# Optimization experiments

Measured on AMD Instinct MI355X. Metric: run time of the kernel, lower is better.

## Reference

```python
import jax, jax.numpy as jnp
import numpy as np

N_HEADS = 16
ROPE_BASE = 10000.0


def _rope(x):
    # x: [B, L, H, Dh]; LLaMA-style rotate-half RoPE, applied over seq dim 1
    B, L, H, Dh = x.shape
    half = Dh // 2
    inv_freq = 1.0 / (ROPE_BASE ** (jnp.arange(0, half, dtype=jnp.float32) / half))
    ang = jnp.arange(L, dtype=jnp.float32)[:, None] * inv_freq[None, :]  # [L, half]
    cos = jnp.concatenate([jnp.cos(ang), jnp.cos(ang)], axis=-1).astype(x.dtype)  # [L, Dh]
    sin = jnp.concatenate([jnp.sin(ang), jnp.sin(ang)], axis=-1).astype(x.dtype)
    cos = cos[None, :, None, :]
    sin = sin[None, :, None, :]
    x1, x2 = x[..., :half], x[..., half:]
    rot = jnp.concatenate([-x2, x1], axis=-1)
    return x * cos + rot * sin


def setup_inputs() -> dict:
    key = jax.random.key(0)
    k1, k2, k3 = jax.random.split(key, 3)
    B, L, D = 2, 2048, 1024
    x = jax.random.normal(k1, (B, L, D), dtype=jnp.float32)
    w_qkv = jax.random.normal(k2, (3 * D, D), dtype=jnp.float32) * (D ** -0.5)
    w_out = jax.random.normal(k3, (D, D), dtype=jnp.float32) * (D ** -0.5)
    return {"x": x, "w_qkv": w_qkv, "w_out": w_out}


def reference(x, w_qkv, w_out):
    B, L, D = x.shape
    H = N_HEADS
    Dh = D // H
    qkv = jnp.einsum('bld,ed->ble', x, w_qkv)  # [B, L, 3D]
    q, k, v = jnp.split(qkv, 3, axis=-1)
    q = q.reshape(B, L, H, Dh)
    k = k.reshape(B, L, H, Dh)
    v = v.reshape(B, L, H, Dh)
    q = _rope(q)
    k = _rope(k)
    scale = 1.0 / jnp.sqrt(jnp.asarray(Dh, dtype=x.dtype))
    scores = jnp.einsum('blhd,bmhd->bhlm', q, k) * scale  # [B, H, L, L]
    attn = jax.nn.softmax(scores, axis=-1)
    out = jnp.einsum('bhlm,bmhd->blhd', attn, v).reshape(B, L, D)
    return jnp.einsum('bld,ed->ble', out, w_out)
```

## Files before the change

### kernel.cpp

```cpp
#include <hip/hip_runtime.h>
#include <hip/hip_bf16.h>
#include <stdint.h>


typedef __attribute__((ext_vector_type(8))) short short8;
typedef __attribute__((ext_vector_type(4))) float floatx4;
typedef __attribute__((ext_vector_type(16))) float floatx16;
typedef __attribute__((ext_vector_type(4))) int intx4;

#define BDIM 2
#define LDIM 2048
#define DDIM 1024
#define HDIM 16
#define DH 64
#define ML (BDIM * LDIM)

#define QSCALE 0.18033688011112042f
#define SMBIAS 16.0f

__device__ __forceinline__ uint16_t f2b(float x) {
  uint32_t b = __float_as_uint(x);
  b += 0x7FFFu + ((b >> 16) & 1u);
  return (uint16_t)(b >> 16);
}

__device__ __forceinline__ uint32_t pack2(float a, float b) {
  return (uint32_t)f2b(a) | ((uint32_t)f2b(b) << 16);
}

__device__ __forceinline__ uint32_t cvtpk(float lo, float hi) {
  uint32_t r;
  asm("v_cvt_pk_bf16_f32 %0, %1, %2" : "=v"(r) : "v"(lo), "v"(hi));
  return r;
}

#define PLSWAP(a, b) asm("v_permlane32_swap_b32 %0, %1" : "+v"(a), "+v"(b))

__device__ __forceinline__ void load_lds_16B(const uint16_t* g, uint16_t* l) {
  __builtin_amdgcn_global_load_lds(
      (const __attribute__((address_space(1))) void*)g,
      (__attribute__((address_space(3))) void*)l, 16, 0, 0);
}

#define WAIT_BAR(N) do {                                         \
    asm volatile("s_waitcnt vmcnt(" #N ")" ::: "memory");        \
    __builtin_amdgcn_sched_barrier(0);                           \
    __builtin_amdgcn_s_barrier();                                \
    asm volatile("" ::: "memory");                               \
    __builtin_amdgcn_sched_barrier(0);                           \
  } while (0)

union I4S8 { intx4 i; short8 s; };

__global__ void prep(const float* __restrict__ x, const float* __restrict__ wqkv,
                     const float* __restrict__ wout,
                     uint16_t* __restrict__ xb, uint16_t* __restrict__ wqkvb,
                     uint16_t* __restrict__ woutb,
                     float* __restrict__ cosT, float* __restrict__ sinT) {
  const int N0 = ML * DDIM / 4;
  const int N1 = 3 * DDIM * DDIM / 4;
  const int N2 = DDIM * DDIM / 4;
  int id = blockIdx.x * 256 + threadIdx.x;
  if (id < N0) {
    float4 v = ((const float4*)x)[id];
    ((uint2*)xb)[id] = make_uint2(pack2(v.x, v.y), pack2(v.z, v.w));
  } else if (id < N0 + N1) {
    int i = id - N0;
    float4 v = ((const float4*)wqkv)[i];
    ((uint2*)wqkvb)[i] = make_uint2(pack2(v.x, v.y), pack2(v.z, v.w));
  } else if (id < N0 + N1 + N2) {
    int i = id - N0 - N1;
    float4 v = ((const float4*)wout)[i];
    ((uint2*)woutb)[i] = make_uint2(pack2(v.x, v.y), pack2(v.z, v.w));
  } else {
    int i = id - N0 - N1 - N2;
    int l = i >> 5, f = i & 31;
    float invf = exp2f(-(float)f * (13.287712379549449f / 32.f));
    float ang = (float)l * invf;
    cosT[i] = cosf(ang);
    sinT[i] = sinf(ang);
  }
}

__device__ __forceinline__ void gemm_step(const uint16_t* __restrict__ as,
                                          const uint16_t* __restrict__ bs,
                                          int wr, int wc, int c0, int c1,
                                          floatx4 (&acc)[4][4]) {
  short8 a[4], b[4];
#pragma unroll
  for (int i = 0; i < 4; ++i)
    a[i] = *(const short8*)&as[(wr * 64 + i * 16 + c0) * 32 + c1 * 8];
#pragma unroll
  for (int j = 0; j < 4; ++j)
    b[j] = *(const short8*)&bs[(wc * 64 + j * 16 + c0) * 32 + c1 * 8];
#pragma unroll
  for (int i = 0; i < 4; ++i)
#pragma unroll
    for (int j = 0; j < 4; ++j)
      acc[i][j] = __builtin_amdgcn_mfma_f32_16x16x32_bf16(a[i], b[j], acc[i][j], 0, 0, 0);
}

#define GEMM_STAGE(BUF, K0) do {                                              \
    const uint16_t* ga = A + (size_t)(m0 + srow) * K + (K0) + scol;           \
    load_lds_16B(ga, &As[(BUF) * 4096 + t * 8]);                              \
    load_lds_16B(ga + (size_t)64 * K, &As[(BUF) * 4096 + 2048 + t * 8]);      \
    const uint16_t* gb = Bm + (size_t)(n0 + srow) * K + (K0) + scol;          \
    load_lds_16B(gb, &Bs[(BUF) * 4096 + t * 8]);                              \
    load_lds_16B(gb + (size_t)64 * K, &Bs[(BUF) * 4096 + 2048 + t * 8]);      \
  } while (0)

__global__ __launch_bounds__(256) void gemm_bt(const uint16_t* __restrict__ A,
                                               const uint16_t* __restrict__ Bm,
                                               float* __restrict__ C,
                                               int M, int N, int K) {
  __shared__ uint16_t As[3 * 4096];
  __shared__ uint16_t Bs[3 * 4096];
  const int m0 = blockIdx.x * 128;
  const int n0 = blockIdx.y * 128;
  const int t = threadIdx.x;
  const int lane = t & 63;
  const int w = t >> 6;
  const int wr = w >> 1, wc = w & 1;
  const int srow = t >> 2;
  const int scol = (t & 3) * 8;
  const int c0 = lane & 15, c1 = lane >> 4;

  floatx4 acc[4][4];
#pragma unroll
  for (int i = 0; i < 4; ++i)
#pragma unroll
    for (int j = 0; j < 4; ++j) acc[i][j] = (floatx4){0.f, 0.f, 0.f, 0.f};

  const int nk = K >> 5;
  GEMM_STAGE(0, 0);
  GEMM_STAGE(1, 32);
#pragma unroll 1
  for (int ki = 0; ki < nk - 1; ++ki) {
    WAIT_BAR(4);
    if (ki + 2 < nk) GEMM_STAGE((ki + 2) % 3, (ki + 2) * 32);
    gemm_step(&As[(ki % 3) * 4096], &Bs[(ki % 3) * 4096], wr, wc, c0, c1, acc);
  }
  WAIT_BAR(0);
  gemm_step(&As[((nk - 1) % 3) * 4096], &Bs[((nk - 1) % 3) * 4096], wr, wc, c0, c1, acc);

#pragma unroll
  for (int i = 0; i < 4; ++i)
#pragma unroll
    for (int j = 0; j < 4; ++j) {
      int row = m0 + wr * 64 + i * 16 + c1 * 4;
      int col = n0 + wc * 64 + j * 16 + c0;
      float* cp = C + (size_t)row * N + col;
#pragma unroll
      for (int r = 0; r < 4; ++r) cp[(size_t)r * N] = acc[i][j][r];
    }
}

__global__ __launch_bounds__(256) void gemm_qkv_rope(const uint16_t* __restrict__ A,
                                                     const uint16_t* __restrict__ Bm,
                                                     const float* __restrict__ cosT,
                                                     const float* __restrict__ sinT,
                                                     uint16_t* __restrict__ qr,
                                                     uint16_t* __restrict__ kr,
                                                     uint16_t* __restrict__ vT) {
  constexpr int K = DDIM;
  __shared__ uint16_t As[3 * 4096];
  __shared__ uint16_t Bs[3 * 4096];
  const int m0 = blockIdx.x * 128;
  const int n0 = blockIdx.y * 128;
  const int t = threadIdx.x;
  const int lane = t & 63;
  const int w = t >> 6;
  const int wr = w >> 1, wc = w & 1;
  const int srow = t >> 2;
  const int scol = (t & 3) * 8;
  const int c0 = lane & 15, c1 = lane >> 4;

  floatx4 acc[4][4];
#pragma unroll
  for (int i = 0; i < 4; ++i)
#pragma unroll
    for (int j = 0; j < 4; ++j) acc[i][j] = (floatx4){0.f, 0.f, 0.f, 0.f};

  const int nk = K >> 5;
  GEMM_STAGE(0, 0);
  GEMM_STAGE(1, 32);
#pragma unroll 1
  for (int ki = 0; ki < nk - 1; ++ki) {
    WAIT_BAR(4);
    if (ki + 2 < nk) GEMM_STAGE((ki + 2) % 3, (ki + 2) * 32);
    gemm_step(&As[(ki % 3) * 4096], &Bs[(ki % 3) * 4096], wr, wc, c0, c1, acc);
  }
  WAIT_BAR(0);
  gemm_step(&As[((nk - 1) % 3) * 4096], &Bs[((nk - 1) % 3) * 4096], wr, wc, c0, c1, acc);

#pragma unroll
  for (int j = 0; j < 4; ++j) {
    const int col = n0 + wc * 64 + j * 16 + c0;
    const int sec = col >> 10;
    const int e = col & 1023;
    const int h = e >> 6, dh = e & 63;
#pragma unroll
    for (int i = 0; i < 4; ++i) {
      const int row = m0 + wr * 64 + i * 16 + c1 * 4;
      const int bb = row >> 11;
      const int l = row & 2047;
      if (sec == 2) {
        uint16_t* vp = vT + ((size_t)((bb * HDIM + h) * DH + dh)) * LDIM + l;
#pragma unroll
        for (int r = 0; r < 4; ++r) vp[r] = f2b(acc[i][j][r]);
      } else {
        const float sgn = (dh < 32) ? -1.f : 1.f;
        const float sc = (sec == 0) ? QSCALE : 1.f;
        uint16_t* dp = (sec == 0 ? qr : kr) + ((size_t)((bb * HDIM + h) * LDIM + l)) * DH + dh;
        const int fi = l * 32 + (dh & 31);
#pragma unroll
        for (int r = 0; r < 4; ++r) {
          float cv = cosT[fi + r * 32];
          float sv = sinT[fi + r * 32];
          float o = (acc[i][j][r] * cv + sgn * acc[i][j ^ 2][r] * sv) * sc;
          dp[(size_t)r * DH] = f2b(o);
        }
      }
    }
  }
}


__device__ __forceinline__ void qk_phase(const uint16_t* __restrict__ kt,
                                         const int (&off)[2][4],
                                         const short8 (&qb)[4],
                                         floatx16& s0, floatx16& s1) {
  floatx16 z = (floatx16){-SMBIAS,-SMBIAS,-SMBIAS,-SMBIAS,-SMBIAS,-SMBIAS,-SMBIAS,-SMBIAS,
                          -SMBIAS,-SMBIAS,-SMBIAS,-SMBIAS,-SMBIAS,-SMBIAS,-SMBIAS,-SMBIAS};
  s0 = z; s1 = z;
  __builtin_amdgcn_s_setprio(1);
#pragma unroll
  for (int c = 0; c < 4; ++c) {
    short8 ka = *(const short8*)(kt + off[0][c]);
    s0 = __builtin_amdgcn_mfma_f32_32x32x16_bf16(ka, qb[c], s0, 0, 0, 0);
  }
#pragma unroll
  for (int c = 0; c < 4; ++c) {
    short8 ka = *(const short8*)(kt + off[1][c]);
    s1 = __builtin_amdgcn_mfma_f32_32x32x16_bf16(ka, qb[c], s1, 0, 0, 0);
  }
  __builtin_amdgcn_s_setprio(0);
}

__device__ __forceinline__ void sm_pv(const uint16_t* __restrict__ vt,
                                      const int (&off)[2][4],
                                      floatx16& s0, floatx16& s1,
                                      float& lsum,
                                      floatx16& acc0, floatx16& acc1) {
  float e[32];
#pragma unroll
  for (int r = 0; r < 16; ++r) e[r] = __builtin_amdgcn_exp2f(s0[r]);
#pragma unroll
  for (int r = 0; r < 16; ++r) e[16 + r] = __builtin_amdgcn_exp2f(s1[r]);
  float ts0 = 0.f, ts1 = 0.f, ts2 = 0.f, ts3 = 0.f;
#pragma unroll
  for (int r = 0; r < 8; ++r) {
    ts0 += e[r]; ts1 += e[8 + r]; ts2 += e[16 + r]; ts3 += e[24 + r];
  }
  lsum += (ts0 + ts1) + (ts2 + ts3);

  uint32_t w0 = cvtpk(e[0], e[1]),   w1 = cvtpk(e[2], e[3]);
  uint32_t w2 = cvtpk(e[4], e[5]),   w3 = cvtpk(e[6], e[7]);
  uint32_t w4 = cvtpk(e[8], e[9]),   w5 = cvtpk(e[10], e[11]);
  uint32_t w6 = cvtpk(e[12], e[13]), w7 = cvtpk(e[14], e[15]);
  uint32_t w8 = cvtpk(e[16], e[17]), w9 = cvtpk(e[18], e[19]);
  uint32_t wa = cvtpk(e[20], e[21]), wb = cvtpk(e[22], e[23]);
  uint32_t wc_ = cvtpk(e[24], e[25]), wd = cvtpk(e[26], e[27]);
  uint32_t we = cvtpk(e[28], e[29]), wf = cvtpk(e[30], e[31]);
  PLSWAP(w0, w2);  PLSWAP(w1, w3);
  PLSWAP(w4, w6);  PLSWAP(w5, w7);
  PLSWAP(w8, wa);  PLSWAP(w9, wb);
  PLSWAP(wc_, we); PLSWAP(wd, wf);
  I4S8 pf0, pf1, pf2, pf3;
  pf0.i = (intx4){(int)w0, (int)w1, (int)w2, (int)w3};
  pf1.i = (intx4){(int)w4, (int)w5, (int)w6, (int)w7};
  pf2.i = (intx4){(int)w8, (int)w9, (int)wa, (int)wb};
  pf3.i = (intx4){(int)wc_, (int)wd, (int)we, (int)wf};

  __builtin_amdgcn_s_setprio(1);
#pragma unroll
  for (int d = 0; d < 2; ++d) {
    floatx16& ac = d ? acc1 : acc0;
    ac = __builtin_amdgcn_mfma_f32_32x32x16_bf16(*(const short8*)(vt + off[d][0]), pf0.s, ac, 0, 0, 0);
    ac = __builtin_amdgcn_mfma_f32_32x32x16_bf16(*(const short8*)(vt + off[d][1]), pf1.s, ac, 0, 0, 0);
    ac = __builtin_amdgcn_mfma_f32_32x32x16_bf16(*(const short8*)(vt + off[d][2]), pf2.s, ac, 0, 0, 0);
    ac = __builtin_amdgcn_mfma_f32_32x32x16_bf16(*(const short8*)(vt + off[d][3]), pf3.s, ac, 0, 0, 0);
  }
  __builtin_amdgcn_s_setprio(0);
}

__global__ __launch_bounds__(256) void attn(const uint16_t* __restrict__ qr,
                                            const uint16_t* __restrict__ kr,
                                            const uint16_t* __restrict__ vT,
                                            uint16_t* __restrict__ out) {
  __shared__ uint16_t KsA[4 * 4096];
  __shared__ uint16_t VsA[4 * 4096];
  const int t = threadIdx.x, lane = t & 63, w = t >> 6;
  const int l31 = lane & 31, hi = lane >> 5;

  const int id = blockIdx.x;
  const int sw = (id & 7) * 64 + (id >> 3);
  const int bx = sw & 15;
  const int h = (sw >> 4) & 15;
  const int b = sw >> 8;

  const int bh = b * HDIM + h;
  const uint16_t* Qb = qr + (size_t)bh * LDIM * DH;
  const char* Kp = (const char*)(kr + (size_t)bh * LDIM * DH);
  const char* Vp = (const char*)(vT + (size_t)bh * DH * LDIM);

  const int srow = t >> 3;
  const int scsw = ((t & 7) * 16) ^ ((srow & 7) << 4);
  const char* kgs = Kp + (size_t)srow * 128 + scsw;
  const char* vgs = Vp + (size_t)srow * (LDIM * 2) + scsw;

#define STAGE(BUF, N) do {                                                     \
    uint16_t* kd = &KsA[(BUF) * 4096];                                         \
    uint16_t* vd = &VsA[(BUF) * 4096];                                         \
    load_lds_16B((const uint16_t*)(kgs + (size_t)(N) * 8192), &kd[t * 8]);     \
    load_lds_16B((const uint16_t*)(kgs + (size_t)(N) * 8192 + 4096), &kd[2048 + t * 8]); \
    load_lds_16B((const uint16_t*)(vgs + (size_t)(N) * 128), &vd[t * 8]);      \
    load_lds_16B((const uint16_t*)(vgs + (size_t)(N) * 128 + 2 * 32 * LDIM), &vd[2048 + t * 8]); \
  } while (0)

  const int q0 = bx * 128 + w * 32;
  short8 qb[4];
#pragma unroll
  for (int c = 0; c < 4; ++c)
    qb[c] = *(const short8*)&Qb[(size_t)(q0 + l31) * DH + c * 16 + hi * 8];

  const int swz = (l31 & 7) << 4;
  int off[2][4];
#pragma unroll
  for (int x = 0; x < 2; ++x)
#pragma unroll
    for (int c = 0; c < 4; ++c)
      off[x][c] = (x * 32 + l31) * 64 + (((c * 32 + hi * 16) ^ swz) >> 1);

  float lsum = 0.f;
  floatx16 acc0 = (floatx16){0.f,0.f,0.f,0.f,0.f,0.f,0.f,0.f,0.f,0.f,0.f,0.f,0.f,0.f,0.f,0.f};
  floatx16 acc1 = acc0;
  floatx16 sA0, sA1, sB0, sB1;

  STAGE(0, 0); STAGE(1, 1); STAGE(2, 2);
  WAIT_BAR(8);
  qk_phase(&KsA[0], off, qb, sA0, sA1);

#define BODY(n, CS0, CS1, NS0, NS1, WN) do {                                   \
    WAIT_BAR(WN);                                                              \
    if ((n) + 3 < 32) STAGE(((n) + 3) & 3, (n) + 3);                           \
    qk_phase(&KsA[(((n) + 1) & 3) * 4096], off, qb, NS0, NS1);                 \
    sm_pv(&VsA[((n) & 3) * 4096], off, CS0, CS1, lsum, acc0, acc1);            \
  } while (0)

#pragma unroll 1
  for (int n = 0; n < 30; n += 2) {
    BODY(n, sA0, sA1, sB0, sB1, 4);
    BODY(n + 1, sB0, sB1, sA0, sA1, 4);
  }
  BODY(30, sA0, sA1, sB0, sB1, 0);
  sm_pv(&VsA[3 * 4096], off, sB0, sB1, lsum, acc0, acc1);
#undef BODY
#undef STAGE

  float ltot = lsum + __shfl_xor(lsum, 32);
  float inv = 1.f / ltot;
  size_t orow = (size_t)(b * LDIM) + bx * 128 + w * 32 + l31;
  uint16_t* op = out + orow * DDIM + h * DH;
#pragma unroll
  for (int g = 0; g < 4; ++g) {
    *(uint2*)&op[8 * g + 4 * hi] =
        make_uint2(cvtpk(acc0[4 * g] * inv, acc0[4 * g + 1] * inv),
                   cvtpk(acc0[4 * g + 2] * inv, acc0[4 * g + 3] * inv));
    *(uint2*)&op[32 + 8 * g + 4 * hi] =
        make_uint2(cvtpk(acc1[4 * g] * inv, acc1[4 * g + 1] * inv),
                   cvtpk(acc1[4 * g + 2] * inv, acc1[4 * g + 3] * inv));
  }
}

static constexpr size_t OFF_XB    = 0;
static constexpr size_t OFF_WQKVB = (size_t)8 << 20;
static constexpr size_t OFF_WOUTB = (size_t)14 << 20;
static constexpr size_t OFF_QR    = (size_t)16 << 20;
static constexpr size_t OFF_KR    = (size_t)24 << 20;
static constexpr size_t OFF_VT    = (size_t)32 << 20;
static constexpr size_t OFF_AO    = (size_t)40 << 20;
static constexpr size_t OFF_COS   = (size_t)48 << 20;
static constexpr size_t OFF_SIN   = OFF_COS + ((size_t)256 << 10);

extern "C" void kernel_launch(void* const* d_in, const int* in_sizes, int n_in,
                              void* d_out, int out_size, void* d_ws, size_t ws_size,
                              hipStream_t stream) {
  const float* x     = (const float*)d_in[0];
  const float* w_qkv = (const float*)d_in[1];
  const float* w_out = (const float*)d_in[2];
  float* out = (float*)d_out;
  char* ws = (char*)d_ws;

  uint16_t* xb    = (uint16_t*)(ws + OFF_XB);
  uint16_t* wqkvb = (uint16_t*)(ws + OFF_WQKVB);
  uint16_t* woutb = (uint16_t*)(ws + OFF_WOUTB);
  uint16_t* qr    = (uint16_t*)(ws + OFF_QR);
  uint16_t* kr    = (uint16_t*)(ws + OFF_KR);
  uint16_t* vT    = (uint16_t*)(ws + OFF_VT);
  uint16_t* ao    = (uint16_t*)(ws + OFF_AO);
  float*    cosT  = (float*)(ws + OFF_COS);
  float*    sinT  = (float*)(ws + OFF_SIN);

  prep<<<8448, 256, 0, stream>>>(x, w_qkv, w_out, xb, wqkvb, woutb, cosT, sinT);

  gemm_qkv_rope<<<dim3(ML / 128, 3 * DDIM / 128), 256, 0, stream>>>(xb, wqkvb, cosT, sinT, qr, kr, vT);

  attn<<<512, 256, 0, stream>>>(qr, kr, vT, ao);

  gemm_bt<<<dim3(ML / 128, DDIM / 128), 256, 0, stream>>>(ao, woutb, out, ML, DDIM, DDIM);
}
```

Before: 116.0 us.

## Stage QKV epilogue through LDS for coalesced stores and swizzle GEMM block order

The QKV+RoPE GEMM epilogue now writes results into a padded shared-memory tile and then emits 16-byte coalesced stores to q, k and the transposed v, replacing scattered 2-byte global writes. Both GEMMs switch to a 1D grid with an XCD-aware block swizzle (id&7 mapping), so blocks sharing an A or B panel land on the same chiplet for better L2 reuse. The cost is extra LDS traffic and two barriers in the epilogue. The swizzle hardcodes the grid shapes (32 row tiles).

```diff
diff --git a/kernel.cpp b/kernel.cpp
--- a/kernel.cpp
+++ b/kernel.cpp
@@ -115,8 +115,10 @@
                                                int M, int N, int K) {
   __shared__ uint16_t As[3 * 4096];
   __shared__ uint16_t Bs[3 * 4096];
-  const int m0 = blockIdx.x * 128;
-  const int n0 = blockIdx.y * 128;
+  const int id = blockIdx.x;
+  const int sw = (id & 7) * (gridDim.x >> 3) + (id >> 3);
+  const int m0 = (sw & 31) * 128;
+  const int n0 = (sw >> 5) * 128;
   const int t = threadIdx.x;
   const int lane = t & 63;
   const int w = t >> 6;
@@ -163,10 +165,13 @@
                                                      uint16_t* __restrict__ kr,
                                                      uint16_t* __restrict__ vT) {
   constexpr int K = DDIM;
-  __shared__ uint16_t As[3 * 4096];
-  __shared__ uint16_t Bs[3 * 4096];
-  const int m0 = blockIdx.x * 128;
-  const int n0 = blockIdx.y * 128;
+  __shared__ uint16_t SH[6 * 4096];
+  uint16_t* As = SH;
+  uint16_t* Bs = SH + 3 * 4096;
+  const int id = blockIdx.x;
+  const int sw = (id & 7) * 96 + (id >> 3);
+  const int m0 = (sw & 31) * 128;
+  const int n0 = (sw >> 5) * 128;
   const int t = threadIdx.x;
   const int lane = t & 63;
   const int w = t >> 6;
@@ -193,35 +198,62 @@
   WAIT_BAR(0);
   gemm_step(&As[((nk - 1) % 3) * 4096], &Bs[((nk - 1) % 3) * 4096], wr, wc, c0, c1, acc);
 
-#pragma unroll
-  for (int j = 0; j < 4; ++j) {
-    const int col = n0 + wc * 64 + j * 16 + c0;
-    const int sec = col >> 10;
-    const int e = col & 1023;
-    const int h = e >> 6, dh = e & 63;
-#pragma unroll
-    for (int i = 0; i < 4; ++i) {
-      const int row = m0 + wr * 64 + i * 16 + c1 * 4;
-      const int bb = row >> 11;
-      const int l = row & 2047;
-      if (sec == 2) {
-        uint16_t* vp = vT + ((size_t)((bb * HDIM + h) * DH + dh)) * LDIM + l;
-#pragma unroll
-        for (int r = 0; r < 4; ++r) vp[r] = f2b(acc[i][j][r]);
-      } else {
-        const float sgn = (dh < 32) ? -1.f : 1.f;
-        const float sc = (sec == 0) ? QSCALE : 1.f;
-        uint16_t* dp = (sec == 0 ? qr : kr) + ((size_t)((bb * HDIM + h) * LDIM + l)) * DH + dh;
-        const int fi = l * 32 + (dh & 31);
+  __syncthreads();
+  uint16_t (*ep)[136] = (uint16_t (*)[136])SH;
+  const int sec = n0 >> 10;
+  const int bb = m0 >> 11;
+  const int l0 = m0 & 2047;
+
+  if (sec == 2) {
+#pragma unroll
+    for (int j = 0; j < 4; ++j) {
+      const int colL = wc * 64 + j * 16 + c0;
+#pragma unroll
+      for (int i = 0; i < 4; ++i) {
+        const int rowL = wr * 64 + i * 16 + c1 * 4;
+#pragma unroll
+        for (int r = 0; r < 4; ++r)
+          ep[colL][rowL + r] = f2b(acc[i][j][r]);
+      }
+    }
+  } else {
+    const float sc = (sec == 0) ? QSCALE : 1.f;
+#pragma unroll
+    for (int j = 0; j < 4; ++j) {
+      const int colL = wc * 64 + j * 16 + c0;
+      const int dh = colL & 63;
+      const float sgn = (dh < 32) ? -1.f : 1.f;
+#pragma unroll
+      for (int i = 0; i < 4; ++i) {
+        const int rowL = wr * 64 + i * 16 + c1 * 4;
+        const int fi = (l0 + rowL) * 32 + (dh & 31);
 #pragma unroll
         for (int r = 0; r < 4; ++r) {
           float cv = cosT[fi + r * 32];
           float sv = sinT[fi + r * 32];
           float o = (acc[i][j][r] * cv + sgn * acc[i][j ^ 2][r] * sv) * sc;
-          dp[(size_t)r * DH] = f2b(o);
+          ep[rowL + r][colL] = f2b(o);
         }
       }
     }
+  }
+  __syncthreads();
+
+  {
+    const int erow = t >> 1, seg = t & 1;
+    const uint16_t* srcp = &ep[erow][seg * 64];
+    uint16_t* dst;
+    if (sec == 2) {
+      const int h2 = ((n0 - 2048) >> 6) + (erow >> 6);
+      const int dh = erow & 63;
+      dst = vT + ((size_t)((bb * HDIM + h2) * DH + dh)) * LDIM + l0 + seg * 64;
+    } else {
+      const int h2 = ((n0 & 1023) >> 6) + seg;
+      dst = (sec == 0 ? qr : kr) + ((size_t)((bb * HDIM + h2) * LDIM + l0 + erow)) * DH;
+    }
+#pragma unroll
+    for (int q = 0; q < 8; ++q)
+      ((uint4*)dst)[q] = ((const uint4*)srcp)[q];
   }
 }
 
@@ -414,9 +446,9 @@
 
   prep<<<8448, 256, 0, stream>>>(x, w_qkv, w_out, xb, wqkvb, woutb, cosT, sinT);
 
-  gemm_qkv_rope<<<dim3(ML / 128, 3 * DDIM / 128), 256, 0, stream>>>(xb, wqkvb, cosT, sinT, qr, kr, vT);
+  gemm_qkv_rope<<<768, 256, 0, stream>>>(xb, wqkvb, cosT, sinT, qr, kr, vT);
 
   attn<<<512, 256, 0, stream>>>(qr, kr, vT, ao);
 
-  gemm_bt<<<dim3(ML / 128, DDIM / 128), 256, 0, stream>>>(ao, woutb, out, ML, DDIM, DDIM);
-}
+  gemm_bt<<<256, 256, 0, stream>>>(ao, woutb, out, ML, DDIM, DDIM);
+}
```

New measurement: 124.8 us. 7.6% more time.

## Split attention KV range across two blocks with separate reduction kernel

Applied to the files above, without the earlier changes.

The attention kernel now splits each query tile's 32 KV chunks between two blocks (split-K), launching 1024 blocks instead of 512. Each block writes unnormalized fp32 partial outputs and row sums to workspace, and a new attn_norm kernel adds the halves, normalizes and writes bf16. It also drops the software-pipelined QK/PV overlap in favor of a single fused phase and shrinks LDS staging from 4 to 3 buffers. The goal is more blocks to fill the GPU's compute units; the cost is extra fp32 traffic, an additional launch, and losing the QK-softmax overlap.

```diff
diff --git a/kernel.cpp b/kernel.cpp
--- a/kernel.cpp
+++ b/kernel.cpp
@@ -226,13 +226,13 @@
 }
 
 
-__device__ __forceinline__ void qk_phase(const uint16_t* __restrict__ kt,
-                                         const int (&off)[2][4],
-                                         const short8 (&qb)[4],
-                                         floatx16& s0, floatx16& s1) {
-  floatx16 z = (floatx16){-SMBIAS,-SMBIAS,-SMBIAS,-SMBIAS,-SMBIAS,-SMBIAS,-SMBIAS,-SMBIAS,
-                          -SMBIAS,-SMBIAS,-SMBIAS,-SMBIAS,-SMBIAS,-SMBIAS,-SMBIAS,-SMBIAS};
-  s0 = z; s1 = z;
+__device__ __forceinline__ void attn_phase(
+    const uint16_t* __restrict__ kt, const uint16_t* __restrict__ vt,
+    const int (&off)[2][4], const short8 (&qb)[4],
+    float& lsum, floatx16& acc0, floatx16& acc1) {
+  floatx16 s0 = (floatx16){-SMBIAS,-SMBIAS,-SMBIAS,-SMBIAS,-SMBIAS,-SMBIAS,-SMBIAS,-SMBIAS,
+                           -SMBIAS,-SMBIAS,-SMBIAS,-SMBIAS,-SMBIAS,-SMBIAS,-SMBIAS,-SMBIAS};
+  floatx16 s1 = s0;
   __builtin_amdgcn_s_setprio(1);
 #pragma unroll
   for (int c = 0; c < 4; ++c) {
@@ -245,13 +245,7 @@
     s1 = __builtin_amdgcn_mfma_f32_32x32x16_bf16(ka, qb[c], s1, 0, 0, 0);
   }
   __builtin_amdgcn_s_setprio(0);
-}
-
-__device__ __forceinline__ void sm_pv(const uint16_t* __restrict__ vt,
-                                      const int (&off)[2][4],
-                                      floatx16& s0, floatx16& s1,
-                                      float& lsum,
-                                      floatx16& acc0, floatx16& acc1) {
+
   float e[32];
 #pragma unroll
   for (int r = 0; r < 16; ++r) e[r] = __builtin_amdgcn_exp2f(s0[r]);
@@ -297,17 +291,20 @@
 __global__ __launch_bounds__(256) void attn(const uint16_t* __restrict__ qr,
                                             const uint16_t* __restrict__ kr,
                                             const uint16_t* __restrict__ vT,
-                                            uint16_t* __restrict__ out) {
-  __shared__ uint16_t KsA[4 * 4096];
-  __shared__ uint16_t VsA[4 * 4096];
+                                            float* __restrict__ pO,
+                                            float* __restrict__ pL) {
+  __shared__ uint16_t KsA[3 * 4096];
+  __shared__ uint16_t VsA[3 * 4096];
   const int t = threadIdx.x, lane = t & 63, w = t >> 6;
   const int l31 = lane & 31, hi = lane >> 5;
 
   const int id = blockIdx.x;
-  const int sw = (id & 7) * 64 + (id >> 3);
-  const int bx = sw & 15;
-  const int h = (sw >> 4) & 15;
-  const int b = sw >> 8;
+  const int sw = (id & 7) * 128 + (id >> 3);
+  const int kvh = sw & 1;
+  const int rest = sw >> 1;
+  const int bx = rest & 15;
+  const int h = (rest >> 4) & 15;
+  const int b = rest >> 8;
 
   const int bh = b * HDIM + h;
   const uint16_t* Qb = qr + (size_t)bh * LDIM * DH;
@@ -318,6 +315,7 @@
   const int scsw = ((t & 7) * 16) ^ ((srow & 7) << 4);
   const char* kgs = Kp + (size_t)srow * 128 + scsw;
   const char* vgs = Vp + (size_t)srow * (LDIM * 2) + scsw;
+  const int base = kvh * 16;
 
 #define STAGE(BUF, N) do {                                                     \
     uint16_t* kd = &KsA[(BUF) * 4096];                                         \
@@ -345,41 +343,73 @@
   float lsum = 0.f;
   floatx16 acc0 = (floatx16){0.f,0.f,0.f,0.f,0.f,0.f,0.f,0.f,0.f,0.f,0.f,0.f,0.f,0.f,0.f,0.f};
   floatx16 acc1 = acc0;
-  floatx16 sA0, sA1, sB0, sB1;
-
-  STAGE(0, 0); STAGE(1, 1); STAGE(2, 2);
-  WAIT_BAR(8);
-  qk_phase(&KsA[0], off, qb, sA0, sA1);
-
-#define BODY(n, CS0, CS1, NS0, NS1, WN) do {                                   \
-    WAIT_BAR(WN);                                                              \
-    if ((n) + 3 < 32) STAGE(((n) + 3) & 3, (n) + 3);                           \
-    qk_phase(&KsA[(((n) + 1) & 3) * 4096], off, qb, NS0, NS1);                 \
-    sm_pv(&VsA[((n) & 3) * 4096], off, CS0, CS1, lsum, acc0, acc1);            \
-  } while (0)
-
+
+  STAGE(0, base + 0);
+  STAGE(1, base + 1);
 #pragma unroll 1
-  for (int n = 0; n < 30; n += 2) {
-    BODY(n, sA0, sA1, sB0, sB1, 4);
-    BODY(n + 1, sB0, sB1, sA0, sA1, 4);
-  }
-  BODY(30, sA0, sA1, sB0, sB1, 0);
-  sm_pv(&VsA[3 * 4096], off, sB0, sB1, lsum, acc0, acc1);
-#undef BODY
+  for (int n = 0; n < 15; ++n) {
+    WAIT_BAR(4);
+    if (n + 2 < 16) STAGE((n + 2) % 3, base + n + 2);
+    attn_phase(&KsA[(n % 3) * 4096], &VsA[(n % 3) * 4096], off, qb, lsum, acc0, acc1);
+  }
+  WAIT_BAR(0);
+  attn_phase(&KsA[(15 % 3) * 4096], &VsA[(15 % 3) * 4096], off, qb, lsum, acc0, acc1);
 #undef STAGE
 
   float ltot = lsum + __shfl_xor(lsum, 32);
-  float inv = 1.f / ltot;
-  size_t orow = (size_t)(b * LDIM) + bx * 128 + w * 32 + l31;
-  uint16_t* op = out + orow * DDIM + h * DH;
-#pragma unroll
-  for (int g = 0; g < 4; ++g) {
-    *(uint2*)&op[8 * g + 4 * hi] =
-        make_uint2(cvtpk(acc0[4 * g] * inv, acc0[4 * g + 1] * inv),
-                   cvtpk(acc0[4 * g + 2] * inv, acc0[4 * g + 3] * inv));
-    *(uint2*)&op[32 + 8 * g + 4 * hi] =
-        make_uint2(cvtpk(acc1[4 * g] * inv, acc1[4 * g + 1] * inv),
-                   cvtpk(acc1[4 * g + 2] * inv, acc1[4 * g + 3] * inv));
+  {
+    float* po = pO + ((size_t)(rest * 2 + kvh) * 64 + 4 * hi) * 128 + w * 32 + l31;
+#pragma unroll
+    for (int g = 0; g < 4; ++g)
+#pragma unroll
+      for (int r = 0; r < 4; ++r) {
+        po[(8 * g + r) * 128] = acc0[4 * g + r];
+        po[(32 + 8 * g + r) * 128] = acc1[4 * g + r];
+      }
+    if (hi == 0)
+      pL[(rest * 2 + kvh) * 128 + w * 32 + l31] = ltot;
+  }
+}
+
+__global__ __launch_bounds__(256) void attn_norm(const float* __restrict__ pO,
+                                                 const float* __restrict__ pL,
+                                                 uint16_t* __restrict__ ao) {
+  __shared__ float tile[64][132];
+  __shared__ float lt[128];
+  const int rest = blockIdx.x;
+  const int t = threadIdx.x;
+  const int bx = rest & 15, h = (rest >> 4) & 15, b = rest >> 8;
+  const float* p0 = pO + (size_t)(rest * 2) * 8192;
+  const float* p1 = p0 + 8192;
+
+  {
+    const int dh = t >> 2, qq0 = (t & 3) * 32;
+#pragma unroll
+    for (int q = 0; q < 32; q += 4) {
+      float4 a = *(const float4*)&p0[dh * 128 + qq0 + q];
+      float4 c = *(const float4*)&p1[dh * 128 + qq0 + q];
+      tile[dh][qq0 + q + 0] = a.x + c.x;
+      tile[dh][qq0 + q + 1] = a.y + c.y;
+      tile[dh][qq0 + q + 2] = a.z + c.z;
+      tile[dh][qq0 + q + 3] = a.w + c.w;
+    }
+    if (t < 128) lt[t] = pL[(size_t)(rest * 2) * 128 + t] + pL[(size_t)(rest * 2 + 1) * 128 + t];
+  }
+  __syncthreads();
+
+  {
+    const int q = t >> 1, seg = (t & 1) * 32;
+    const float inv = 1.f / lt[q];
+    uint16_t* op = ao + ((size_t)(b * LDIM + bx * 128 + q)) * DDIM + h * DH + seg;
+#pragma unroll
+    for (int d = 0; d < 32; d += 8) {
+      uint4 v;
+      v.x = cvtpk(tile[seg + d + 0][q] * inv, tile[seg + d + 1][q] * inv);
+      v.y = cvtpk(tile[seg + d + 2][q] * inv, tile[seg + d + 3][q] * inv);
+      v.z = cvtpk(tile[seg + d + 4][q] * inv, tile[seg + d + 5][q] * inv);
+      v.w = cvtpk(tile[seg + d + 6][q] * inv, tile[seg + d + 7][q] * inv);
+      *(uint4*)&op[d] = v;
+    }
   }
 }
 
@@ -392,6 +422,8 @@
 static constexpr size_t OFF_AO    = (size_t)40 << 20;
 static constexpr size_t OFF_COS   = (size_t)48 << 20;
 static constexpr size_t OFF_SIN   = OFF_COS + ((size_t)256 << 10);
+static constexpr size_t OFF_PO    = (size_t)56 << 20;
+static constexpr size_t OFF_PL    = (size_t)90 << 20;
 
 extern "C" void kernel_launch(void* const* d_in, const int* in_sizes, int n_in,
                               void* d_out, int out_size, void* d_ws, size_t ws_size,
@@ -411,12 +443,15 @@
   uint16_t* ao    = (uint16_t*)(ws + OFF_AO);
   float*    cosT  = (float*)(ws + OFF_COS);
   float*    sinT  = (float*)(ws + OFF_SIN);
+  float*    pO    = (float*)(ws + OFF_PO);
+  float*    pL    = (float*)(ws + OFF_PL);
 
   prep<<<8448, 256, 0, stream>>>(x, w_qkv, w_out, xb, wqkvb, woutb, cosT, sinT);
 
   gemm_qkv_rope<<<dim3(ML / 128, 3 * DDIM / 128), 256, 0, stream>>>(xb, wqkvb, cosT, sinT, qr, kr, vT);
 
-  attn<<<512, 256, 0, stream>>>(qr, kr, vT, ao);
+  attn<<<1024, 256, 0, stream>>>(qr, kr, vT, pO, pL);
+  attn_norm<<<512, 256, 0, stream>>>(pO, pL, ao);
 
   gemm_bt<<<dim3(ML / 128, DDIM / 128), 256, 0, stream>>>(ao, woutb, out, ML, DDIM, DDIM);
 }
```

After: 132.6 us. 14.4% more time.
